# Optimization experiments

Measured on AMD Instinct MI355X. Metric: run time of the kernel, lower is better.

## Reference

```python
import jax, jax.numpy as jnp
import numpy as np
from jax import lax


def setup_inputs() -> dict:
    key = jax.random.key(0)
    ks = jax.random.split(key, 5)
    D, S, T, B, H = 2, 48, 48, 32, 256
    std = 1.0 / np.sqrt(H)
    return {
        "src_input_seq": jax.random.normal(ks[0], (S, B, H), jnp.float32),
        "trg_input_seq": jax.random.normal(ks[1], (T, B, H), jnp.float32),
        "W": jax.random.uniform(ks[2], (D, H, H), jnp.float32, -std, std),
        "U": jax.random.uniform(ks[3], (D, 2 * H, H), jnp.float32, -std, std),
        "b": jax.random.uniform(ks[4], (D, 1, H), jnp.float32, -std, std),
    }


def _grid_layer(x, y, Wd, Ud, bd):
    # x, y: [S, T, B, H] per-cell inputs for this depth
    S, T, B, H = x.shape
    Ux, Uy = Ud[:H], Ud[H:]  # state = concat([state_x, state_y]) @ U

    def row_step(prev_row_hx, row_inputs):
        # prev_row_hx: [T, B, H] = h_x of row i-1 (state_x); zeros for i == 0
        x_row, y_row = row_inputs  # [T, B, H]

        def cell_step(left_hx, inp):
            # left_hx: [B, H] = h_x of cell (i, j-1) (state_y); zeros for j == 0
            up_hx, x_t, y_t = inp
            temp = up_hx @ Ux + left_hx @ Uy + bd  # [B, H]
            h_x = jnp.tanh(x_t @ Wd + temp)
            h_y = jnp.tanh(y_t @ Wd + temp)
            return h_x, (h_x, h_y)

        _, (hx_row, hy_row) = lax.scan(
            cell_step, jnp.zeros((B, H), x.dtype), (prev_row_hx, x_row, y_row)
        )
        return hx_row, (hx_row, hy_row)

    _, (HX, HY) = lax.scan(row_step, jnp.zeros((T, B, H), x.dtype), (x, y))
    return jnp.stack([HX, HY], axis=2)  # [S, T, 2, B, H]


def reference(src_input_seq, trg_input_seq, W, U, b):
    S, B, H = src_input_seq.shape
    T = trg_input_seq.shape[0]
    depth = W.shape[0]
    # depth-0 inputs: x_t = src[i] (same for all j), y_t = trg[j] (same for all i)
    xs = jnp.broadcast_to(src_input_seq[:, None], (S, T, B, H))
    ys = jnp.broadcast_to(trg_input_seq[None, :], (S, T, B, H))
    outs = []
    for d in range(depth):
        Hd = _grid_layer(xs, ys, W[d], U[d], b[d])  # [S, T, 2, B, H]
        outs.append(Hd)
        xs, ys = Hd[:, :, 0], Hd[:, :, 1]
    return jnp.stack(outs, axis=0)  # [depth, S, T, 2, B, H]
```

## Files before the change

### kernel.cpp

```cpp
#include <hip/hip_runtime.h>
#include <hip/hip_bf16.h>


typedef short short8 __attribute__((ext_vector_type(8)));
typedef float f32x4 __attribute__((ext_vector_type(4)));

static constexpr size_t UF_OFF    = 0;
static constexpr size_t WF_OFF    = 512u * 1024;
static constexpr size_t SRCW_OFF  = 768u * 1024;
static constexpr size_t TRGW_OFF  = SRCW_OFF + 48u * 32 * 256 * 4;
static constexpr size_t FLAG0_OFF = TRGW_OFF + 48u * 32 * 256 * 4;
static constexpr size_t FLAG1_OFF = FLAG0_OFF + 48u * 48 * 128;

#define MFMA16(a, b, c) __builtin_amdgcn_mfma_f32_16x16x32_bf16(a, b, c, 0, 0, 0)

__device__ __forceinline__ short f2bf(float f) {
  __hip_bfloat16 h = __float2bfloat16(f);
  return __builtin_bit_cast(short, h);
}

__device__ __forceinline__ size_t plane_off(int d, int s, int t, int c) {
  return (size_t)(((d * 48 + s) * 48 + t) * 2 + c) * 8192u;
}

__device__ __forceinline__ int* flagp(char* ws, size_t off, int s, int t) {
  return (int*)(ws + off) + (size_t)(s * 48 + t) * 32;
}

__device__ __forceinline__ void wait_ge(int* p, int v) {
  while (__hip_atomic_load(p, __ATOMIC_RELAXED, __HIP_MEMORY_SCOPE_AGENT) < v)
    __builtin_amdgcn_s_sleep(1);
  asm volatile("" ::: "memory");
}

__device__ __forceinline__ void st_llc(float* p, float v) {
  __hip_atomic_store(p, v, __ATOMIC_RELAXED, __HIP_MEMORY_SCOPE_AGENT);
}

__device__ __forceinline__ float fast_tanh(float x) {
  float e = exp2f(x * 2.88539008f);
  return 1.f - __fdividef(2.f, e + 1.f);
}

__global__ void preswizzle(const float* __restrict__ U,
                           const float* __restrict__ W,
                           char* __restrict__ ws) {
  int gid = blockIdx.x * 256 + threadIdx.x;
  if (gid < 32768) {
    int r = gid >> 11;
    int d = r >> 3, nh = (r >> 2) & 1, w = r & 3;
    int c = gid & 2047;
    int f = c >> 6, lane = c & 63;
    int nt = f >> 4, ks = f & 15;
    int kbase = ks * 32 + (lane >> 4) * 8;
    int n = nh * 128 + w * 32 + nt * 16 + (lane & 15);
    const float* sp = U + (size_t)d * 512 * 256 + n;
    short8 v;
#pragma unroll
    for (int j = 0; j < 8; ++j) v[j] = f2bf(sp[(size_t)(kbase + j) * 256]);
    *(short8*)(ws + UF_OFF + (size_t)gid * 16) = v;
  } else {
    int idx = gid - 32768;
    int r = idx >> 10;
    int d = r >> 3, nh = (r >> 2) & 1, w = r & 3;
    int c = idx & 1023;
    int f = c >> 6, lane = c & 63;
    int nt = f >> 3, ks = f & 7;
    int kbase = ks * 32 + (lane >> 4) * 8;
    int n = nh * 128 + w * 32 + nt * 16 + (lane & 15);
    const float* sp = W + (size_t)d * 256 * 256 + n;
    short8 v;
#pragma unroll
    for (int j = 0; j < 8; ++j) v[j] = f2bf(sp[(size_t)(kbase + j) * 256]);
    *(short8*)(ws + WF_OFF + (size_t)idx * 16) = v;
  }
}

__global__ __launch_bounds__(256, 1) void precompute_xw(
    const float* __restrict__ src, const float* __restrict__ trg,
    const float* __restrict__ bvec, char* __restrict__ ws) {
  __shared__ __align__(16) char lds[32 * 528];
  const int bid = blockIdx.x;
  const int i = bid >> 1, nh = bid & 1;
  const int tid = threadIdx.x;
  const int w = tid >> 6, lane = tid & 63;
  const int alane = lane & 15, q = lane >> 4;

  short8 bw[2][8];
  {
    const char* wb = ws + WF_OFF + (size_t)(nh * 4 + w) * 16384u + (size_t)lane * 16;
#pragma unroll
    for (int nt = 0; nt < 2; ++nt)
#pragma unroll
      for (int ks = 0; ks < 8; ++ks)
        bw[nt][ks] = *(const short8*)(wb + (nt * 8 + ks) * 1024);
  }

  const float* plane = (i < 48) ? src + (size_t)i * 8192 : trg + (size_t)(i - 48) * 8192;
#pragma unroll
  for (int it = 0; it < 4; ++it) {
    int gid = it * 256 + tid;
    int row = gid >> 5, c = gid & 31;
    const float* p = plane + row * 256 + c * 8;
    short8 v;
#pragma unroll
    for (int j = 0; j < 8; ++j) v[j] = f2bf(p[j]);
    *(short8*)(lds + row * 528 + c * 16) = v;
  }
  __syncthreads();

  const f32x4 zf = {0.f, 0.f, 0.f, 0.f};
  f32x4 acc[2][2];
  acc[0][0] = zf; acc[0][1] = zf; acc[1][0] = zf; acc[1][1] = zf;
  const char* ar0 = lds + alane * 528 + q * 16;
  const char* ar1 = lds + (alane + 16) * 528 + q * 16;
#pragma unroll
  for (int ks = 0; ks < 8; ++ks) {
    short8 a0 = *(const short8*)(ar0 + ks * 64);
    short8 a1 = *(const short8*)(ar1 + ks * 64);
#pragma unroll
    for (int nt = 0; nt < 2; ++nt) {
      acc[0][nt] = MFMA16(a0, bw[nt][ks], acc[0][nt]);
      acc[1][nt] = MFMA16(a1, bw[nt][ks], acc[1][nt]);
    }
  }

  const int n0 = nh * 128 + w * 32 + alane;
  float bs[2] = {bvec[n0], bvec[n0 + 16]};
  const int gtid = (nh * 4 + w) * 64 + lane;
  float* dst = (float*)(ws + (i < 48 ? SRCW_OFF : TRGW_OFF)) +
               (size_t)(i < 48 ? i : i - 48) * 8192 + (size_t)gtid * 16;
#pragma unroll
  for (int mt = 0; mt < 2; ++mt)
#pragma unroll
    for (int nt = 0; nt < 2; ++nt) {
      f32x4 v = acc[mt][nt];
      v[0] += bs[nt]; v[1] += bs[nt]; v[2] += bs[nt]; v[3] += bs[nt];
      ((f32x4*)dst)[mt * 2 + nt] = v;
    }
}

__global__ __launch_bounds__(512, 1) void grid_main(
    float* __restrict__ out, const float* __restrict__ bvec,
    char* __restrict__ ws) {
  __shared__ __align__(16) char lds[4 * 32 * 528];
  char* const buf0 = lds;
  char* const buf1 = lds + 32 * 528;
  char* const buf2 = lds + 2 * 32 * 528;
  char* const buf3 = lds + 3 * 32 * 528;

  const int bid = blockIdx.x;
  const int d = bid / 48;
  const int t = bid % 48;
  const int tid = threadIdx.x;
  const int wv = tid >> 6;
  const int nh = wv >> 2, w = wv & 3;
  const int lane = tid & 63;
  const int alane = lane & 15, q = lane >> 4;
  const int n0 = nh * 128 + w * 32 + alane;

  const float* SRCW = (const float*)(ws + SRCW_OFF);
  const float* TRGW = (const float*)(ws + TRGW_OFF);

  short8 bu[2][16];
  {
    const char* ub = ws + UF_OFF + (size_t)((d * 2 + nh) * 4 + w) * 32768u +
                     (size_t)lane * 16;
#pragma unroll
    for (int nt = 0; nt < 2; ++nt)
#pragma unroll
      for (int ks = 0; ks < 16; ++ks)
        bu[nt][ks] = *(const short8*)(ub + (nt * 16 + ks) * 1024);
  }

  for (int z = tid; z < 32 * 528 / 4; z += 512) ((int*)buf0)[z] = 0;
  __syncthreads();

  const char* up0 = buf0 + alane * 528 + q * 16;
  const char* up1 = buf0 + (alane + 16) * 528 + q * 16;
  const char* l0  = buf1 + alane * 528 + q * 16;
  const char* l1  = buf1 + (alane + 16) * 528 + q * 16;
  const char* y0  = buf2 + alane * 528 + q * 16;
  const char* y1  = buf2 + (alane + 16) * 528 + q * 16;
  const char* m0  = buf3 + alane * 528 + q * 16;
  const char* m1  = buf3 + (alane + 16) * 528 + q * 16;
  const f32x4 zf = {0.f, 0.f, 0.f, 0.f};

  if (d == 0) {
    f32x4 pfy[4];
    {
      const f32x4* py = (const f32x4*)(TRGW + (size_t)t * 8192 + (size_t)tid * 16);
      pfy[0] = py[0]; pfy[1] = py[1]; pfy[2] = py[2]; pfy[3] = py[3];
    }
    for (int s = 0; s < 48; ++s) {
      f32x4 accx[2][2], accy[2][2], accT[2][2];
      {
        const f32x4* px = (const f32x4*)(SRCW + (size_t)s * 8192 + (size_t)tid * 16);
        accx[0][0] = px[0]; accx[0][1] = px[1]; accx[1][0] = px[2]; accx[1][1] = px[3];
      }
      accy[0][0] = pfy[0]; accy[0][1] = pfy[1]; accy[1][0] = pfy[2]; accy[1][1] = pfy[3];
      accT[0][0] = zf; accT[0][1] = zf; accT[1][0] = zf; accT[1][1] = zf;

      f32x4 lva[2], lvb[2];
      if (t > 0) {
        wait_ge(flagp(ws, FLAG0_OFF, s, t - 1), 8);
        const float* pl = out + plane_off(0, s, t - 1, 0);
#pragma unroll
        for (int it = 0; it < 2; ++it) {
          int gid = it * 512 + tid;
          int row = gid >> 5, c = gid & 31;
          const float* p = pl + row * 256 + c * 8;
          lva[it] = *(const f32x4*)p;
          lvb[it] = *(const f32x4*)(p + 4);
        }
      }
#pragma unroll
      for (int ks = 0; ks < 8; ++ks) {
        short8 a0 = *(const short8*)(up0 + ks * 64);
        short8 a1 = *(const short8*)(up1 + ks * 64);
        accT[0][0] = MFMA16(a0, bu[0][ks], accT[0][0]);
        accT[0][1] = MFMA16(a0, bu[1][ks], accT[0][1]);
        accT[1][0] = MFMA16(a1, bu[0][ks], accT[1][0]);
        accT[1][1] = MFMA16(a1, bu[1][ks], accT[1][1]);
      }
      if (t > 0) {
#pragma unroll
        for (int it = 0; it < 2; ++it) {
          int gid = it * 512 + tid;
          int row = gid >> 5, c = gid & 31;
          short8 v;
#pragma unroll
          for (int j = 0; j < 4; ++j) {
            v[j] = f2bf(lva[it][j]);
            v[4 + j] = f2bf(lvb[it][j]);
          }
          *(short8*)(buf1 + row * 528 + c * 16) = v;
        }
      }
      __syncthreads();
      if (t > 0) {
#pragma unroll
        for (int ks = 0; ks < 8; ++ks) {
          short8 a0 = *(const short8*)(l0 + ks * 64);
          short8 a1 = *(const short8*)(l1 + ks * 64);
          accT[0][0] = MFMA16(a0, bu[0][8 + ks], accT[0][0]);
          accT[0][1] = MFMA16(a0, bu[1][8 + ks], accT[0][1]);
          accT[1][0] = MFMA16(a1, bu[0][8 + ks], accT[1][0]);
          accT[1][1] = MFMA16(a1, bu[1][8 + ks], accT[1][1]);
        }
      }
      float hxv[16];
      {
        float* hxp = out + plane_off(0, s, t, 0);
#pragma unroll
        for (int mt = 0; mt < 2; ++mt)
#pragma unroll
          for (int nt = 0; nt < 2; ++nt)
#pragma unroll
            for (int rr = 0; rr < 4; ++rr) {
              int i = (mt * 2 + nt) * 4 + rr;
              int row = mt * 16 + q * 4 + rr, c = n0 + nt * 16;
              float xv = fast_tanh(accx[mt][nt][rr] + accT[mt][nt][rr]);
              hxv[i] = xv;
              st_llc(&hxp[row * 256 + c], xv);
            }
      }
      asm volatile("s_waitcnt vmcnt(0)" ::: "memory");
      if (lane == 0)
        __hip_atomic_fetch_add(flagp(ws, FLAG0_OFF, s, t), 1,
                               __ATOMIC_RELAXED, __HIP_MEMORY_SCOPE_AGENT);
      {
        float* hyp = out + plane_off(0, s, t, 1);
#pragma unroll
        for (int mt = 0; mt < 2; ++mt)
#pragma unroll
          for (int nt = 0; nt < 2; ++nt)
#pragma unroll
            for (int rr = 0; rr < 4; ++rr) {
              int row = mt * 16 + q * 4 + rr, c = n0 + nt * 16;
              st_llc(&hyp[row * 256 + c],
                     fast_tanh(accy[mt][nt][rr] + accT[mt][nt][rr]));
            }
      }
      asm volatile("s_waitcnt vmcnt(0)" ::: "memory");
      if (lane == 0)
        __hip_atomic_fetch_add(flagp(ws, FLAG0_OFF, s, t) + 1, 1,
                               __ATOMIC_RELAXED, __HIP_MEMORY_SCOPE_AGENT);
#pragma unroll
      for (int mt = 0; mt < 2; ++mt)
#pragma unroll
        for (int nt = 0; nt < 2; ++nt)
#pragma unroll
          for (int rr = 0; rr < 4; ++rr) {
            int row = mt * 16 + q * 4 + rr, c = n0 + nt * 16;
            *(short*)(buf0 + row * 528 + c * 2) = f2bf(hxv[(mt * 2 + nt) * 4 + rr]);
          }
      __syncthreads();
    }
  } else {
    const char* wbp = ws + WF_OFF + (size_t)((2 + nh) * 4 + w) * 16384u +
                      (size_t)lane * 16;
    const float bsa = bvec[256 + n0], bsb = bvec[256 + n0 + 16];
    const f32x4 bA = {bsa, bsa, bsa, bsa};
    const f32x4 bB = {bsb, bsb, bsb, bsb};
    for (int s = 0; s < 48; ++s) {
      f32x4 accx[2][2], accy[2][2], accT[2][2];
      accx[0][0] = bA; accx[0][1] = bB; accx[1][0] = bA; accx[1][1] = bB;
      accy[0][0] = bA; accy[0][1] = bB; accy[1][0] = bA; accy[1][1] = bB;
      accT[0][0] = zf; accT[0][1] = zf; accT[1][0] = zf; accT[1][1] = zf;

      wait_ge(flagp(ws, FLAG0_OFF, s, t) + 1, 8);
      f32x4 xva[4], xvb[4];
      {
        const float* px = out + plane_off(0, s, t, 0);
        const float* py = out + plane_off(0, s, t, 1);
#pragma unroll
        for (int it = 0; it < 4; ++it) {
          int gid = it * 512 + tid;
          int pidx = gid >> 10, row = (gid >> 5) & 31, c = gid & 31;
          const float* pp = (pidx ? py : px) + row * 256 + c * 8;
          xva[it] = *(const f32x4*)pp;
          xvb[it] = *(const f32x4*)(pp + 4);
        }
      }
#pragma unroll
      for (int ks = 0; ks < 8; ++ks) {
        short8 a0 = *(const short8*)(up0 + ks * 64);
        short8 a1 = *(const short8*)(up1 + ks * 64);
        accT[0][0] = MFMA16(a0, bu[0][ks], accT[0][0]);
        accT[0][1] = MFMA16(a0, bu[1][ks], accT[0][1]);
        accT[1][0] = MFMA16(a1, bu[0][ks], accT[1][0]);
        accT[1][1] = MFMA16(a1, bu[1][ks], accT[1][1]);
      }
      {
#pragma unroll
        for (int it = 0; it < 4; ++it) {
          int gid = it * 512 + tid;
          int pidx = gid >> 10, row = (gid >> 5) & 31, c = gid & 31;
          char* db = pidx ? buf2 : buf1;
          short8 v;
#pragma unroll
          for (int j = 0; j < 4; ++j) {
            v[j] = f2bf(xva[it][j]);
            v[4 + j] = f2bf(xvb[it][j]);
          }
          *(short8*)(db + row * 528 + c * 16) = v;
        }
      }
      __syncthreads();
#pragma unroll
      for (int ks = 0; ks < 8; ++ks) {
        short8 b0 = *(const short8*)(wbp + ks * 1024);
        short8 b1 = *(const short8*)(wbp + (8 + ks) * 1024);
        short8 ax0 = *(const short8*)(l0 + ks * 64);
        short8 ax1 = *(const short8*)(l1 + ks * 64);
        short8 ay0 = *(const short8*)(y0 + ks * 64);
        short8 ay1 = *(const short8*)(y1 + ks * 64);
        accx[0][0] = MFMA16(ax0, b0, accx[0][0]);
        accx[0][1] = MFMA16(ax0, b1, accx[0][1]);
        accx[1][0] = MFMA16(ax1, b0, accx[1][0]);
        accx[1][1] = MFMA16(ax1, b1, accx[1][1]);
        accy[0][0] = MFMA16(ay0, b0, accy[0][0]);
        accy[0][1] = MFMA16(ay0, b1, accy[0][1]);
        accy[1][0] = MFMA16(ay1, b0, accy[1][0]);
        accy[1][1] = MFMA16(ay1, b1, accy[1][1]);
      }
      if (t > 0) {
        wait_ge(flagp(ws, FLAG1_OFF, s, t - 1), 8);
        const float* pl = out + plane_off(1, s, t - 1, 0);
        f32x4 lva[2], lvb[2];
#pragma unroll
        for (int it = 0; it < 2; ++it) {
          int gid = it * 512 + tid;
          int row = gid >> 5, c = gid & 31;
          const float* p = pl + row * 256 + c * 8;
          lva[it] = *(const f32x4*)p;
          lvb[it] = *(const f32x4*)(p + 4);
        }
#pragma unroll
        for (int it = 0; it < 2; ++it) {
          int gid = it * 512 + tid;
          int row = gid >> 5, c = gid & 31;
          short8 v;
#pragma unroll
          for (int j = 0; j < 4; ++j) {
            v[j] = f2bf(lva[it][j]);
            v[4 + j] = f2bf(lvb[it][j]);
          }
          *(short8*)(buf3 + row * 528 + c * 16) = v;
        }
      }
      __syncthreads();
      if (t > 0) {
#pragma unroll
        for (int ks = 0; ks < 8; ++ks) {
          short8 a0 = *(const short8*)(m0 + ks * 64);
          short8 a1 = *(const short8*)(m1 + ks * 64);
          accT[0][0] = MFMA16(a0, bu[0][8 + ks], accT[0][0]);
          accT[0][1] = MFMA16(a0, bu[1][8 + ks], accT[0][1]);
          accT[1][0] = MFMA16(a1, bu[0][8 + ks], accT[1][0]);
          accT[1][1] = MFMA16(a1, bu[1][8 + ks], accT[1][1]);
        }
      }
      float hxv[16];
      {
        float* hxp = out + plane_off(1, s, t, 0);
#pragma unroll
        for (int mt = 0; mt < 2; ++mt)
#pragma unroll
          for (int nt = 0; nt < 2; ++nt)
#pragma unroll
            for (int rr = 0; rr < 4; ++rr) {
              int i = (mt * 2 + nt) * 4 + rr;
              int row = mt * 16 + q * 4 + rr, c = n0 + nt * 16;
              float xv = fast_tanh(accx[mt][nt][rr] + accT[mt][nt][rr]);
              hxv[i] = xv;
              st_llc(&hxp[row * 256 + c], xv);
            }
      }
      asm volatile("s_waitcnt vmcnt(0)" ::: "memory");
      if (lane == 0)
        __hip_atomic_fetch_add(flagp(ws, FLAG1_OFF, s, t), 1,
                               __ATOMIC_RELAXED, __HIP_MEMORY_SCOPE_AGENT);
      {
        float* hyp = out + plane_off(1, s, t, 1);
#pragma unroll
        for (int mt = 0; mt < 2; ++mt)
#pragma unroll
          for (int nt = 0; nt < 2; ++nt)
#pragma unroll
            for (int rr = 0; rr < 4; ++rr) {
              int row = mt * 16 + q * 4 + rr, c = n0 + nt * 16;
              hyp[row * 256 + c] =
                  fast_tanh(accy[mt][nt][rr] + accT[mt][nt][rr]);
            }
      }
#pragma unroll
      for (int mt = 0; mt < 2; ++mt)
#pragma unroll
        for (int nt = 0; nt < 2; ++nt)
#pragma unroll
          for (int rr = 0; rr < 4; ++rr) {
            int row = mt * 16 + q * 4 + rr, c = n0 + nt * 16;
            *(short*)(buf0 + row * 528 + c * 2) = f2bf(hxv[(mt * 2 + nt) * 4 + rr]);
          }
      __syncthreads();
    }
  }
}

extern "C" void kernel_launch(void* const* d_in, const int* in_sizes, int n_in,
                              void* d_out, int out_size, void* d_ws, size_t ws_size,
                              hipStream_t stream) {
  const float* src = (const float*)d_in[0];
  const float* trg = (const float*)d_in[1];
  const float* W   = (const float*)d_in[2];
  const float* U   = (const float*)d_in[3];
  const float* bv  = (const float*)d_in[4];
  float* out = (float*)d_out;
  char* ws = (char*)d_ws;

  hipMemsetAsync(ws + FLAG0_OFF, 0, 2u * 48 * 48 * 128, stream);
  preswizzle<<<192, 256, 0, stream>>>(U, W, ws);
  precompute_xw<<<192, 256, 0, stream>>>(src, trg, bv, ws);
  grid_main<<<96, 512, 0, stream>>>(out, bv, ws);
}
```

Baseline: 816.8 us.

## Pass precomputed left-state products between blocks via flagged ring buffer

Each block (one grid column t) now computes both its own next-row up-state product and the left-state product h_x@Uy destined for column t+1. It publishes that product into a 4-deep ring buffer in workspace, with an embedded sequence tag per 16-byte chunk. The consumer polls the tagged data directly instead of waiting on a flag and then converting h_x to bf16 and running its own MFMA. This takes the flag round-trip and the left GEMM off the cross-block critical path, and ACK counters give the producer back-pressure. The cost is extra workspace traffic, a more complex handshake and the risk of ordering bugs.

```diff
diff --git a/kernel.cpp b/kernel.cpp
--- a/kernel.cpp
+++ b/kernel.cpp
@@ -4,13 +4,18 @@
 
 typedef short short8 __attribute__((ext_vector_type(8)));
 typedef float f32x4 __attribute__((ext_vector_type(4)));
+typedef int   i32x4 __attribute__((ext_vector_type(4)));
 
 static constexpr size_t UF_OFF    = 0;
 static constexpr size_t WF_OFF    = 512u * 1024;
 static constexpr size_t SRCW_OFF  = 768u * 1024;
 static constexpr size_t TRGW_OFF  = SRCW_OFF + 48u * 32 * 256 * 4;
 static constexpr size_t FLAG0_OFF = TRGW_OFF + 48u * 32 * 256 * 4;
-static constexpr size_t FLAG1_OFF = FLAG0_OFF + 48u * 48 * 128;
+static constexpr size_t P0_OFF    = FLAG0_OFF + 48u * 48 * 128;
+static constexpr size_t P1_OFF    = P0_OFF + 48u * 4 * 49152;
+static constexpr size_t ACK0_OFF  = P1_OFF + 48u * 4 * 49152;
+static constexpr size_t ACK1_OFF  = ACK0_OFF + 48u * 8 * 128;
+static constexpr size_t WS_END    = ACK1_OFF + 48u * 8 * 128;
 
 #define MFMA16(a, b, c) __builtin_amdgcn_mfma_f32_16x16x32_bf16(a, b, c, 0, 0, 0)
 
@@ -21,10 +26,6 @@
 
 __device__ __forceinline__ size_t plane_off(int d, int s, int t, int c) {
   return (size_t)(((d * 48 + s) * 48 + t) * 2 + c) * 8192u;
-}
-
-__device__ __forceinline__ int* flagp(char* ws, size_t off, int s, int t) {
-  return (int*)(ws + off) + (size_t)(s * 48 + t) * 32;
 }
 
 __device__ __forceinline__ void wait_ge(int* p, int v) {
@@ -34,6 +35,9 @@
 }
 
 __device__ __forceinline__ void st_llc(float* p, float v) {
+  __hip_atomic_store(p, v, __ATOMIC_RELAXED, __HIP_MEMORY_SCOPE_AGENT);
+}
+__device__ __forceinline__ void st_llc_i(int* p, int v) {
   __hip_atomic_store(p, v, __ATOMIC_RELAXED, __HIP_MEMORY_SCOPE_AGENT);
 }
 
@@ -143,11 +147,10 @@
 __global__ __launch_bounds__(512, 1) void grid_main(
     float* __restrict__ out, const float* __restrict__ bvec,
     char* __restrict__ ws) {
-  __shared__ __align__(16) char lds[4 * 32 * 528];
+  __shared__ __align__(16) char lds[3 * 32 * 528];
   char* const buf0 = lds;
   char* const buf1 = lds + 32 * 528;
   char* const buf2 = lds + 2 * 32 * 528;
-  char* const buf3 = lds + 3 * 32 * 528;
 
   const int bid = blockIdx.x;
   const int d = bid / 48;
@@ -161,6 +164,8 @@
 
   const float* SRCW = (const float*)(ws + SRCW_OFF);
   const float* TRGW = (const float*)(ws + TRGW_OFF);
+  const size_t POFF = d ? P1_OFF : P0_OFF;
+  int* const ACK = (int*)(ws + (d ? ACK1_OFF : ACK0_OFF));
 
   short8 bu[2][16];
   {
@@ -173,18 +178,18 @@
         bu[nt][ks] = *(const short8*)(ub + (nt * 16 + ks) * 1024);
   }
 
-  for (int z = tid; z < 32 * 528 / 4; z += 512) ((int*)buf0)[z] = 0;
-  __syncthreads();
-
   const char* up0 = buf0 + alane * 528 + q * 16;
   const char* up1 = buf0 + (alane + 16) * 528 + q * 16;
-  const char* l0  = buf1 + alane * 528 + q * 16;
-  const char* l1  = buf1 + (alane + 16) * 528 + q * 16;
+  const char* x0  = buf1 + alane * 528 + q * 16;
+  const char* x1  = buf1 + (alane + 16) * 528 + q * 16;
   const char* y0  = buf2 + alane * 528 + q * 16;
   const char* y1  = buf2 + (alane + 16) * 528 + q * 16;
-  const char* m0  = buf3 + alane * 528 + q * 16;
-  const char* m1  = buf3 + (alane + 16) * 528 + q * 16;
   const f32x4 zf = {0.f, 0.f, 0.f, 0.f};
+
+  f32x4 accTup[2][2];
+  accTup[0][0] = zf; accTup[0][1] = zf; accTup[1][0] = zf; accTup[1][1] = zf;
+
+  __syncthreads();
 
   if (d == 0) {
     f32x4 pfy[4];
@@ -193,99 +198,65 @@
       pfy[0] = py[0]; pfy[1] = py[1]; pfy[2] = py[2]; pfy[3] = py[3];
     }
     for (int s = 0; s < 48; ++s) {
-      f32x4 accx[2][2], accy[2][2], accT[2][2];
+      f32x4 sxv[4];
       {
         const f32x4* px = (const f32x4*)(SRCW + (size_t)s * 8192 + (size_t)tid * 16);
-        accx[0][0] = px[0]; accx[0][1] = px[1]; accx[1][0] = px[2]; accx[1][1] = px[3];
-      }
-      accy[0][0] = pfy[0]; accy[0][1] = pfy[1]; accy[1][0] = pfy[2]; accy[1][1] = pfy[3];
-      accT[0][0] = zf; accT[0][1] = zf; accT[1][0] = zf; accT[1][1] = zf;
-
-      f32x4 lva[2], lvb[2];
+        sxv[0] = px[0]; sxv[1] = px[1]; sxv[2] = px[2]; sxv[3] = px[3];
+      }
+      if (t < 47 && s >= 4) wait_ge(ACK + (t * 8 + wv) * 32, s - 3);
+
+      float pv[16];
       if (t > 0) {
-        wait_ge(flagp(ws, FLAG0_OFF, s, t - 1), 8);
-        const float* pl = out + plane_off(0, s, t - 1, 0);
-#pragma unroll
-        for (int it = 0; it < 2; ++it) {
-          int gid = it * 512 + tid;
-          int row = gid >> 5, c = gid & 31;
-          const float* p = pl + row * 256 + c * 8;
-          lva[it] = *(const f32x4*)p;
-          lvb[it] = *(const f32x4*)(p + 4);
+        const char* pb = ws + POFF + ((size_t)(t - 1) * 4 + (size_t)(s & 3)) * 49152u +
+                         (size_t)tid * 96u;
+        const int want = s + 1;
+        f32x4 k0, k1, k2, k3, k4, k5;
+        for (;;) {
+          asm volatile(
+              "global_load_dwordx4 %0, %6, off sc0 sc1\n\t"
+              "global_load_dwordx4 %1, %6, off offset:16 sc0 sc1\n\t"
+              "global_load_dwordx4 %2, %6, off offset:32 sc0 sc1\n\t"
+              "global_load_dwordx4 %3, %6, off offset:48 sc0 sc1\n\t"
+              "global_load_dwordx4 %4, %6, off offset:64 sc0 sc1\n\t"
+              "global_load_dwordx4 %5, %6, off offset:80 sc0 sc1\n\t"
+              "s_waitcnt vmcnt(0)"
+              : "=v"(k0), "=v"(k1), "=v"(k2), "=v"(k3), "=v"(k4), "=v"(k5)
+              : "v"(pb)
+              : "memory");
+          __builtin_amdgcn_sched_barrier(0);
+          i32x4 e0 = __builtin_bit_cast(i32x4, k0), e1 = __builtin_bit_cast(i32x4, k1),
+                e2 = __builtin_bit_cast(i32x4, k2), e3 = __builtin_bit_cast(i32x4, k3),
+                e4 = __builtin_bit_cast(i32x4, k4), e5 = __builtin_bit_cast(i32x4, k5);
+          if (e0.w == want && e1.w == want && e2.w == want &&
+              e3.w == want && e4.w == want && e5.w == want) break;
+          __builtin_amdgcn_s_sleep(1);
         }
-      }
-#pragma unroll
-      for (int ks = 0; ks < 8; ++ks) {
-        short8 a0 = *(const short8*)(up0 + ks * 64);
-        short8 a1 = *(const short8*)(up1 + ks * 64);
-        accT[0][0] = MFMA16(a0, bu[0][ks], accT[0][0]);
-        accT[0][1] = MFMA16(a0, bu[1][ks], accT[0][1]);
-        accT[1][0] = MFMA16(a1, bu[0][ks], accT[1][0]);
-        accT[1][1] = MFMA16(a1, bu[1][ks], accT[1][1]);
-      }
-      if (t > 0) {
-#pragma unroll
-        for (int it = 0; it < 2; ++it) {
-          int gid = it * 512 + tid;
-          int row = gid >> 5, c = gid & 31;
-          short8 v;
-#pragma unroll
-          for (int j = 0; j < 4; ++j) {
-            v[j] = f2bf(lva[it][j]);
-            v[4 + j] = f2bf(lvb[it][j]);
+        pv[0] = k0.x;  pv[1] = k0.y;  pv[2] = k0.z;
+        pv[3] = k1.x;  pv[4] = k1.y;  pv[5] = k1.z;
+        pv[6] = k2.x;  pv[7] = k2.y;  pv[8] = k2.z;
+        pv[9] = k3.x;  pv[10] = k3.y; pv[11] = k3.z;
+        pv[12] = k4.x; pv[13] = k4.y; pv[14] = k4.z;
+        pv[15] = k5.x;
+        if (lane == 0) st_llc_i(ACK + ((t - 1) * 8 + wv) * 32, s + 1);
+      } else {
+#pragma unroll
+        for (int i = 0; i < 16; ++i) pv[i] = 0.f;
+      }
+
+      f32x4 accT[2][2];
+      float hxv[16];
+#pragma unroll
+      for (int mt = 0; mt < 2; ++mt)
+#pragma unroll
+        for (int nt = 0; nt < 2; ++nt)
+#pragma unroll
+          for (int rr = 0; rr < 4; ++rr) {
+            int i = (mt * 2 + nt) * 4 + rr;
+            float tv = accTup[mt][nt][rr] + pv[i];
+            accT[mt][nt][rr] = tv;
+            hxv[i] = fast_tanh(sxv[mt * 2 + nt][rr] + tv);
           }
-          *(short8*)(buf1 + row * 528 + c * 16) = v;
-        }
-      }
       __syncthreads();
-      if (t > 0) {
-#pragma unroll
-        for (int ks = 0; ks < 8; ++ks) {
-          short8 a0 = *(const short8*)(l0 + ks * 64);
-          short8 a1 = *(const short8*)(l1 + ks * 64);
-          accT[0][0] = MFMA16(a0, bu[0][8 + ks], accT[0][0]);
-          accT[0][1] = MFMA16(a0, bu[1][8 + ks], accT[0][1]);
-          accT[1][0] = MFMA16(a1, bu[0][8 + ks], accT[1][0]);
-          accT[1][1] = MFMA16(a1, bu[1][8 + ks], accT[1][1]);
-        }
-      }
-      float hxv[16];
-      {
-        float* hxp = out + plane_off(0, s, t, 0);
-#pragma unroll
-        for (int mt = 0; mt < 2; ++mt)
-#pragma unroll
-          for (int nt = 0; nt < 2; ++nt)
-#pragma unroll
-            for (int rr = 0; rr < 4; ++rr) {
-              int i = (mt * 2 + nt) * 4 + rr;
-              int row = mt * 16 + q * 4 + rr, c = n0 + nt * 16;
-              float xv = fast_tanh(accx[mt][nt][rr] + accT[mt][nt][rr]);
-              hxv[i] = xv;
-              st_llc(&hxp[row * 256 + c], xv);
-            }
-      }
-      asm volatile("s_waitcnt vmcnt(0)" ::: "memory");
-      if (lane == 0)
-        __hip_atomic_fetch_add(flagp(ws, FLAG0_OFF, s, t), 1,
-                               __ATOMIC_RELAXED, __HIP_MEMORY_SCOPE_AGENT);
-      {
-        float* hyp = out + plane_off(0, s, t, 1);
-#pragma unroll
-        for (int mt = 0; mt < 2; ++mt)
-#pragma unroll
-          for (int nt = 0; nt < 2; ++nt)
-#pragma unroll
-            for (int rr = 0; rr < 4; ++rr) {
-              int row = mt * 16 + q * 4 + rr, c = n0 + nt * 16;
-              st_llc(&hyp[row * 256 + c],
-                     fast_tanh(accy[mt][nt][rr] + accT[mt][nt][rr]));
-            }
-      }
-      asm volatile("s_waitcnt vmcnt(0)" ::: "memory");
-      if (lane == 0)
-        __hip_atomic_fetch_add(flagp(ws, FLAG0_OFF, s, t) + 1, 1,
-                               __ATOMIC_RELAXED, __HIP_MEMORY_SCOPE_AGENT);
 #pragma unroll
       for (int mt = 0; mt < 2; ++mt)
 #pragma unroll
@@ -296,6 +267,69 @@
             *(short*)(buf0 + row * 528 + c * 2) = f2bf(hxv[(mt * 2 + nt) * 4 + rr]);
           }
       __syncthreads();
+
+      f32x4 accP[2][2];
+      accP[0][0] = zf; accP[0][1] = zf; accP[1][0] = zf; accP[1][1] = zf;
+      accTup[0][0] = zf; accTup[0][1] = zf; accTup[1][0] = zf; accTup[1][1] = zf;
+#pragma unroll
+      for (int ks = 0; ks < 8; ++ks) {
+        short8 a0 = *(const short8*)(up0 + ks * 64);
+        short8 a1 = *(const short8*)(up1 + ks * 64);
+        accTup[0][0] = MFMA16(a0, bu[0][ks], accTup[0][0]);
+        accTup[0][1] = MFMA16(a0, bu[1][ks], accTup[0][1]);
+        accTup[1][0] = MFMA16(a1, bu[0][ks], accTup[1][0]);
+        accTup[1][1] = MFMA16(a1, bu[1][ks], accTup[1][1]);
+        accP[0][0] = MFMA16(a0, bu[0][8 + ks], accP[0][0]);
+        accP[0][1] = MFMA16(a0, bu[1][8 + ks], accP[0][1]);
+        accP[1][0] = MFMA16(a1, bu[0][8 + ks], accP[1][0]);
+        accP[1][1] = MFMA16(a1, bu[1][8 + ks], accP[1][1]);
+      }
+      if (t < 47) {
+        float pp[16];
+#pragma unroll
+        for (int mt = 0; mt < 2; ++mt)
+#pragma unroll
+          for (int nt = 0; nt < 2; ++nt)
+#pragma unroll
+            for (int rr = 0; rr < 4; ++rr)
+              pp[(mt * 2 + nt) * 4 + rr] = accP[mt][nt][rr];
+        const float ef = __builtin_bit_cast(float, s + 1);
+        f32x4 q0 = {pp[0], pp[1], pp[2], ef},  q1 = {pp[3], pp[4], pp[5], ef};
+        f32x4 q2 = {pp[6], pp[7], pp[8], ef},  q3 = {pp[9], pp[10], pp[11], ef};
+        f32x4 q4 = {pp[12], pp[13], pp[14], ef}, q5 = {pp[15], ef, ef, ef};
+        char* qb = ws + POFF + ((size_t)t * 4 + (size_t)(s & 3)) * 49152u +
+                   (size_t)tid * 96u;
+        asm volatile(
+            "global_store_dwordx4 %6, %0, off sc0 sc1\n\t"
+            "global_store_dwordx4 %6, %1, off offset:16 sc0 sc1\n\t"
+            "global_store_dwordx4 %6, %2, off offset:32 sc0 sc1\n\t"
+            "global_store_dwordx4 %6, %3, off offset:48 sc0 sc1\n\t"
+            "global_store_dwordx4 %6, %4, off offset:64 sc0 sc1\n\t"
+            "global_store_dwordx4 %6, %5, off offset:80 sc0 sc1\n\t"
+            "s_waitcnt vmcnt(0)"
+            :: "v"(q0), "v"(q1), "v"(q2), "v"(q3), "v"(q4), "v"(q5), "v"(qb)
+            : "memory");
+      }
+      {
+        float* hxp = out + plane_off(0, s, t, 0);
+        float* hyp = out + plane_off(0, s, t, 1);
+#pragma unroll
+        for (int mt = 0; mt < 2; ++mt)
+#pragma unroll
+          for (int nt = 0; nt < 2; ++nt)
+#pragma unroll
+            for (int rr = 0; rr < 4; ++rr) {
+              int i = (mt * 2 + nt) * 4 + rr;
+              int row = mt * 16 + q * 4 + rr, c = n0 + nt * 16;
+              float yv = fast_tanh(pfy[mt * 2 + nt][rr] + accT[mt][nt][rr]);
+              st_llc(&hxp[row * 256 + c], hxv[i]);
+              st_llc(&hyp[row * 256 + c], yv);
+            }
+      }
+      asm volatile("s_waitcnt vmcnt(0)" ::: "memory");
+      if (lane == 0)
+        __hip_atomic_fetch_add((int*)(ws + FLAG0_OFF) + (size_t)(s * 48 + t) * 32, 1,
+                               __ATOMIC_RELAXED, __HIP_MEMORY_SCOPE_AGENT);
     }
   } else {
     const char* wbp = ws + WF_OFF + (size_t)((2 + nh) * 4 + w) * 16384u +
@@ -304,12 +338,8 @@
     const f32x4 bA = {bsa, bsa, bsa, bsa};
     const f32x4 bB = {bsb, bsb, bsb, bsb};
     for (int s = 0; s < 48; ++s) {
-      f32x4 accx[2][2], accy[2][2], accT[2][2];
-      accx[0][0] = bA; accx[0][1] = bB; accx[1][0] = bA; accx[1][1] = bB;
-      accy[0][0] = bA; accy[0][1] = bB; accy[1][0] = bA; accy[1][1] = bB;
-      accT[0][0] = zf; accT[0][1] = zf; accT[1][0] = zf; accT[1][1] = zf;
-
-      wait_ge(flagp(ws, FLAG0_OFF, s, t) + 1, 8);
+      if (t < 47 && s >= 4) wait_ge(ACK + (t * 8 + wv) * 32, s - 3);
+      wait_ge((int*)(ws + FLAG0_OFF) + (size_t)(s * 48 + t) * 32, 8);
       f32x4 xva[4], xvb[4];
       {
         const float* px = out + plane_off(0, s, t, 0);
@@ -324,36 +354,28 @@
         }
       }
 #pragma unroll
-      for (int ks = 0; ks < 8; ++ks) {
-        short8 a0 = *(const short8*)(up0 + ks * 64);
-        short8 a1 = *(const short8*)(up1 + ks * 64);
-        accT[0][0] = MFMA16(a0, bu[0][ks], accT[0][0]);
-        accT[0][1] = MFMA16(a0, bu[1][ks], accT[0][1]);
-        accT[1][0] = MFMA16(a1, bu[0][ks], accT[1][0]);
-        accT[1][1] = MFMA16(a1, bu[1][ks], accT[1][1]);
-      }
-      {
-#pragma unroll
-        for (int it = 0; it < 4; ++it) {
-          int gid = it * 512 + tid;
-          int pidx = gid >> 10, row = (gid >> 5) & 31, c = gid & 31;
-          char* db = pidx ? buf2 : buf1;
-          short8 v;
-#pragma unroll
-          for (int j = 0; j < 4; ++j) {
-            v[j] = f2bf(xva[it][j]);
-            v[4 + j] = f2bf(xvb[it][j]);
-          }
-          *(short8*)(db + row * 528 + c * 16) = v;
+      for (int it = 0; it < 4; ++it) {
+        int gid = it * 512 + tid;
+        int pidx = gid >> 10, row = (gid >> 5) & 31, c = gid & 31;
+        char* db = pidx ? buf2 : buf1;
+        short8 v;
+#pragma unroll
+        for (int j = 0; j < 4; ++j) {
+          v[j] = f2bf(xva[it][j]);
+          v[4 + j] = f2bf(xvb[it][j]);
         }
+        *(short8*)(db + row * 528 + c * 16) = v;
       }
       __syncthreads();
+      f32x4 accx[2][2], accy[2][2];
+      accx[0][0] = bA; accx[0][1] = bB; accx[1][0] = bA; accx[1][1] = bB;
+      accy[0][0] = bA; accy[0][1] = bB; accy[1][0] = bA; accy[1][1] = bB;
 #pragma unroll
       for (int ks = 0; ks < 8; ++ks) {
         short8 b0 = *(const short8*)(wbp + ks * 1024);
         short8 b1 = *(const short8*)(wbp + (8 + ks) * 1024);
-        short8 ax0 = *(const short8*)(l0 + ks * 64);
-        short8 ax1 = *(const short8*)(l1 + ks * 64);
+        short8 ax0 = *(const short8*)(x0 + ks * 64);
+        short8 ax1 = *(const short8*)(x1 + ks * 64);
         short8 ay0 = *(const short8*)(y0 + ks * 64);
         short8 ay1 = *(const short8*)(y1 + ks * 64);
         accx[0][0] = MFMA16(ax0, b0, accx[0][0]);
@@ -365,76 +387,58 @@
         accy[1][0] = MFMA16(ay1, b0, accy[1][0]);
         accy[1][1] = MFMA16(ay1, b1, accy[1][1]);
       }
+      float pv[16];
       if (t > 0) {
-        wait_ge(flagp(ws, FLAG1_OFF, s, t - 1), 8);
-        const float* pl = out + plane_off(1, s, t - 1, 0);
-        f32x4 lva[2], lvb[2];
-#pragma unroll
-        for (int it = 0; it < 2; ++it) {
-          int gid = it * 512 + tid;
-          int row = gid >> 5, c = gid & 31;
-          const float* p = pl + row * 256 + c * 8;
-          lva[it] = *(const f32x4*)p;
-          lvb[it] = *(const f32x4*)(p + 4);
+        const char* pb = ws + POFF + ((size_t)(t - 1) * 4 + (size_t)(s & 3)) * 49152u +
+                         (size_t)tid * 96u;
+        const int want = s + 1;
+        f32x4 k0, k1, k2, k3, k4, k5;
+        for (;;) {
+          asm volatile(
+              "global_load_dwordx4 %0, %6, off sc0 sc1\n\t"
+              "global_load_dwordx4 %1, %6, off offset:16 sc0 sc1\n\t"
+              "global_load_dwordx4 %2, %6, off offset:32 sc0 sc1\n\t"
+              "global_load_dwordx4 %3, %6, off offset:48 sc0 sc1\n\t"
+              "global_load_dwordx4 %4, %6, off offset:64 sc0 sc1\n\t"
+              "global_load_dwordx4 %5, %6, off offset:80 sc0 sc1\n\t"
+              "s_waitcnt vmcnt(0)"
+              : "=v"(k0), "=v"(k1), "=v"(k2), "=v"(k3), "=v"(k4), "=v"(k5)
+              : "v"(pb)
+              : "memory");
+          __builtin_amdgcn_sched_barrier(0);
+          i32x4 e0 = __builtin_bit_cast(i32x4, k0), e1 = __builtin_bit_cast(i32x4, k1),
+                e2 = __builtin_bit_cast(i32x4, k2), e3 = __builtin_bit_cast(i32x4, k3),
+                e4 = __builtin_bit_cast(i32x4, k4), e5 = __builtin_bit_cast(i32x4, k5);
+          if (e0.w == want && e1.w == want && e2.w == want &&
+              e3.w == want && e4.w == want && e5.w == want) break;
+          __builtin_amdgcn_s_sleep(1);
         }
-#pragma unroll
-        for (int it = 0; it < 2; ++it) {
-          int gid = it * 512 + tid;
-          int row = gid >> 5, c = gid & 31;
-          short8 v;
-#pragma unroll
-          for (int j = 0; j < 4; ++j) {
-            v[j] = f2bf(lva[it][j]);
-            v[4 + j] = f2bf(lvb[it][j]);
+        pv[0] = k0.x;  pv[1] = k0.y;  pv[2] = k0.z;
+        pv[3] = k1.x;  pv[4] = k1.y;  pv[5] = k1.z;
+        pv[6] = k2.x;  pv[7] = k2.y;  pv[8] = k2.z;
+        pv[9] = k3.x;  pv[10] = k3.y; pv[11] = k3.z;
+        pv[12] = k4.x; pv[13] = k4.y; pv[14] = k4.z;
+        pv[15] = k5.x;
+        if (lane == 0) st_llc_i(ACK + ((t - 1) * 8 + wv) * 32, s + 1);
+      } else {
+#pragma unroll
+        for (int i = 0; i < 16; ++i) pv[i] = 0.f;
+      }
+
+      f32x4 accT[2][2];
+      float hxv[16];
+#pragma unroll
+      for (int mt = 0; mt < 2; ++mt)
+#pragma unroll
+        for (int nt = 0; nt < 2; ++nt)
+#pragma unroll
+          for (int rr = 0; rr < 4; ++rr) {
+            int i = (mt * 2 + nt) * 4 + rr;
+            float tv = accTup[mt][nt][rr] + pv[i];
+            accT[mt][nt][rr] = tv;
+            hxv[i] = fast_tanh(accx[mt][nt][rr] + tv);
           }
-          *(short8*)(buf3 + row * 528 + c * 16) = v;
-        }
-      }
       __syncthreads();
-      if (t > 0) {
-#pragma unroll
-        for (int ks = 0; ks < 8; ++ks) {
-          short8 a0 = *(const short8*)(m0 + ks * 64);
-          short8 a1 = *(const short8*)(m1 + ks * 64);
-          accT[0][0] = MFMA16(a0, bu[0][8 + ks], accT[0][0]);
-          accT[0][1] = MFMA16(a0, bu[1][8 + ks], accT[0][1]);
-          accT[1][0] = MFMA16(a1, bu[0][8 + ks], accT[1][0]);
-          accT[1][1] = MFMA16(a1, bu[1][8 + ks], accT[1][1]);
-        }
-      }
-      float hxv[16];
-      {
-        float* hxp = out + plane_off(1, s, t, 0);
-#pragma unroll
-        for (int mt = 0; mt < 2; ++mt)
-#pragma unroll
-          for (int nt = 0; nt < 2; ++nt)
-#pragma unroll
-            for (int rr = 0; rr < 4; ++rr) {
-              int i = (mt * 2 + nt) * 4 + rr;
-              int row = mt * 16 + q * 4 + rr, c = n0 + nt * 16;
-              float xv = fast_tanh(accx[mt][nt][rr] + accT[mt][nt][rr]);
-              hxv[i] = xv;
-              st_llc(&hxp[row * 256 + c], xv);
-            }
-      }
-      asm volatile("s_waitcnt vmcnt(0)" ::: "memory");
-      if (lane == 0)
-        __hip_atomic_fetch_add(flagp(ws, FLAG1_OFF, s, t), 1,
-                               __ATOMIC_RELAXED, __HIP_MEMORY_SCOPE_AGENT);
-      {
-        float* hyp = out + plane_off(1, s, t, 1);
-#pragma unroll
-        for (int mt = 0; mt < 2; ++mt)
-#pragma unroll
-          for (int nt = 0; nt < 2; ++nt)
-#pragma unroll
-            for (int rr = 0; rr < 4; ++rr) {
-              int row = mt * 16 + q * 4 + rr, c = n0 + nt * 16;
-              hyp[row * 256 + c] =
-                  fast_tanh(accy[mt][nt][rr] + accT[mt][nt][rr]);
-            }
-      }
 #pragma unroll
       for (int mt = 0; mt < 2; ++mt)
 #pragma unroll
@@ -445,6 +449,63 @@
             *(short*)(buf0 + row * 528 + c * 2) = f2bf(hxv[(mt * 2 + nt) * 4 + rr]);
           }
       __syncthreads();
+      f32x4 accP[2][2];
+      accP[0][0] = zf; accP[0][1] = zf; accP[1][0] = zf; accP[1][1] = zf;
+      accTup[0][0] = zf; accTup[0][1] = zf; accTup[1][0] = zf; accTup[1][1] = zf;
+#pragma unroll
+      for (int ks = 0; ks < 8; ++ks) {
+        short8 a0 = *(const short8*)(up0 + ks * 64);
+        short8 a1 = *(const short8*)(up1 + ks * 64);
+        accTup[0][0] = MFMA16(a0, bu[0][ks], accTup[0][0]);
+        accTup[0][1] = MFMA16(a0, bu[1][ks], accTup[0][1]);
+        accTup[1][0] = MFMA16(a1, bu[0][ks], accTup[1][0]);
+        accTup[1][1] = MFMA16(a1, bu[1][ks], accTup[1][1]);
+        accP[0][0] = MFMA16(a0, bu[0][8 + ks], accP[0][0]);
+        accP[0][1] = MFMA16(a0, bu[1][8 + ks], accP[0][1]);
+        accP[1][0] = MFMA16(a1, bu[0][8 + ks], accP[1][0]);
+        accP[1][1] = MFMA16(a1, bu[1][8 + ks], accP[1][1]);
+      }
+      if (t < 47) {
+        float pp[16];
+#pragma unroll
+        for (int mt = 0; mt < 2; ++mt)
+#pragma unroll
+          for (int nt = 0; nt < 2; ++nt)
+#pragma unroll
+            for (int rr = 0; rr < 4; ++rr)
+              pp[(mt * 2 + nt) * 4 + rr] = accP[mt][nt][rr];
+        const float ef = __builtin_bit_cast(float, s + 1);
+        f32x4 q0 = {pp[0], pp[1], pp[2], ef},  q1 = {pp[3], pp[4], pp[5], ef};
+        f32x4 q2 = {pp[6], pp[7], pp[8], ef},  q3 = {pp[9], pp[10], pp[11], ef};
+        f32x4 q4 = {pp[12], pp[13], pp[14], ef}, q5 = {pp[15], ef, ef, ef};
+        char* qb = ws + POFF + ((size_t)t * 4 + (size_t)(s & 3)) * 49152u +
+                   (size_t)tid * 96u;
+        asm volatile(
+            "global_store_dwordx4 %6, %0, off sc0 sc1\n\t"
+            "global_store_dwordx4 %6, %1, off offset:16 sc0 sc1\n\t"
+            "global_store_dwordx4 %6, %2, off offset:32 sc0 sc1\n\t"
+            "global_store_dwordx4 %6, %3, off offset:48 sc0 sc1\n\t"
+            "global_store_dwordx4 %6, %4, off offset:64 sc0 sc1\n\t"
+            "global_store_dwordx4 %6, %5, off offset:80 sc0 sc1\n\t"
+            "s_waitcnt vmcnt(0)"
+            :: "v"(q0), "v"(q1), "v"(q2), "v"(q3), "v"(q4), "v"(q5), "v"(qb)
+            : "memory");
+      }
+      {
+        float* hxp = out + plane_off(1, s, t, 0);
+        float* hyp = out + plane_off(1, s, t, 1);
+#pragma unroll
+        for (int mt = 0; mt < 2; ++mt)
+#pragma unroll
+          for (int nt = 0; nt < 2; ++nt)
+#pragma unroll
+            for (int rr = 0; rr < 4; ++rr) {
+              int i = (mt * 2 + nt) * 4 + rr;
+              int row = mt * 16 + q * 4 + rr, c = n0 + nt * 16;
+              hxp[row * 256 + c] = hxv[i];
+              hyp[row * 256 + c] = fast_tanh(accy[mt][nt][rr] + accT[mt][nt][rr]);
+            }
+      }
     }
   }
 }
@@ -460,7 +521,7 @@
   float* out = (float*)d_out;
   char* ws = (char*)d_ws;
 
-  hipMemsetAsync(ws + FLAG0_OFF, 0, 2u * 48 * 48 * 128, stream);
+  hipMemsetAsync(ws + FLAG0_OFF, 0, WS_END - FLAG0_OFF, stream);
   preswizzle<<<192, 256, 0, stream>>>(U, W, ws);
   precompute_xw<<<192, 256, 0, stream>>>(src, trg, bv, ws);
   grid_main<<<96, 512, 0, stream>>>(out, bv, ws);
```

Result: slower. 1.382 ms (+69.2%).
